# Kernel tuning notes

Measured on AMD Instinct MI355X. Metric: run time of the kernel, lower is better.

The kernel has to match this reference:

```python
import jax, jax.numpy as jnp
import numpy as np

B, P, D = 8, 1024, 1024
H, N = 16, 64  # num_heads, head_dim


def setup_inputs() -> dict:
    key = jax.random.key(0)
    k1, k2, k3 = jax.random.split(key, 3)
    inputs = jax.random.normal(k1, (B, P, D), dtype=jnp.float32)
    # Keras 'random_normal' initializer: stddev 0.05
    w_qkv = jax.random.normal(k2, (H, 3, D, N), dtype=jnp.float32) * 0.05
    w_o = jax.random.normal(k3, (N * H, D), dtype=jnp.float32) * 0.05
    return {"inputs": inputs, "w_qkv": w_qkv, "w_o": w_o}


def reference(inputs, w_qkv, w_o):
    # Per-head QKV projection: [b,p,d] x [h,3,d,n] -> [b,h,3,p,n]
    proj = jnp.einsum('bpv,havn->bhapn', inputs, w_qkv)
    q = proj[:, :, 0]  # [b,h,p,n]
    k = proj[:, :, 1]
    v = proj[:, :, 2]
    head_dim = q.shape[-1]
    scale = 1.0 / jnp.sqrt(jnp.asarray(head_dim, dtype=jnp.float32))
    scores = jnp.einsum('bhqn,bhkn->bhqk', q, k) * scale  # [b,h,p,p]
    attn = jax.nn.softmax(scores, axis=-1)
    out = jnp.einsum('bhqk,bhkn->bhqn', attn, v)  # [b,h,p,n]
    # concat heads along feature dim: [b,p,h*n]
    b, h, p, n = out.shape
    concat = out.transpose(0, 2, 1, 3).reshape(b, p, h * n)
    return jnp.einsum('bpi,ij->bpj', concat, w_o)  # [b,p,d_model]
```

## Files before the change

### kernel.cpp

```cpp
#include <hip/hip_runtime.h>
#include <stdint.h>

typedef _Float16 f16;
typedef __attribute__((ext_vector_type(4))) _Float16 f16x4;
typedef __attribute__((ext_vector_type(8))) _Float16 f16x8;
typedef __attribute__((ext_vector_type(4))) float f32x4;

__device__ __forceinline__ void gload_lds16(const void* g, void* l) {
  __builtin_amdgcn_global_load_lds(
      (__attribute__((address_space(1))) void*)const_cast<void*>(g),
      (__attribute__((address_space(3))) void*)l, 16, 0, 0);
}


__global__ void convert_x(const float* __restrict__ in, f16* __restrict__ out) {
  int i = blockIdx.x * 256 + threadIdx.x;
  float4 v = ((const float4*)in)[i];
  f16x4 hv;
  hv[0] = (f16)v.x; hv[1] = (f16)v.y; hv[2] = (f16)v.z; hv[3] = (f16)v.w;
  ((f16x4*)out)[i] = hv;
}

__global__ void transpose_wqkv(const float* __restrict__ in, f16* __restrict__ out) {
  __shared__ float tile[64][65];
  int s = blockIdx.x >> 4;
  int vt = blockIdx.x & 15;
  int tx = threadIdx.x & 63, ty = threadIdx.x >> 6;
#pragma unroll
  for (int i = 0; i < 16; i++) {
    int r = i * 4 + ty;
    tile[r][tx] = in[((size_t)(s * 1024 + vt * 64 + r)) * 64 + tx];
  }
  __syncthreads();
#pragma unroll
  for (int i = 0; i < 16; i++) {
    int n = i * 4 + ty;
    out[((size_t)(s * 64 + n)) * 1024 + vt * 64 + tx] = (f16)tile[tx][n];
  }
}

__global__ void transpose_wo(const float* __restrict__ in, f16* __restrict__ out) {
  __shared__ float tile[64][65];
  int rt = blockIdx.x >> 4, ct = blockIdx.x & 15;
  int tx = threadIdx.x & 63, ty = threadIdx.x >> 6;
#pragma unroll
  for (int i = 0; i < 16; i++) {
    int r = i * 4 + ty;
    tile[r][tx] = in[((size_t)(rt * 64 + r)) * 1024 + ct * 64 + tx];
  }
  __syncthreads();
#pragma unroll
  for (int i = 0; i < 16; i++) {
    int j = i * 4 + ty;
    out[((size_t)(ct * 64 + j)) * 1024 + rt * 64 + tx] = (f16)tile[tx][j];
  }
}

__global__ void transpose_v(const f16* __restrict__ QKV, f16* __restrict__ VT) {
  __shared__ f16 tile[64][65];
  int bh = blockIdx.x >> 4, pt = blockIdx.x & 15;
  int b = bh >> 4, h = bh & 15;
  int tx = threadIdx.x & 63, ty = threadIdx.x >> 6;
#pragma unroll
  for (int i = 0; i < 16; i++) {
    int r = i * 4 + ty;
    tile[r][tx] = QKV[((size_t)(b * 1024 + pt * 64 + r)) * 3072 + h * 192 + 128 + tx];
  }
  __syncthreads();
#pragma unroll
  for (int i = 0; i < 16; i++) {
    int n = i * 4 + ty;
    VT[((size_t)(bh * 64 + n)) * 1024 + pt * 64 + tx] = tile[tx][n];
  }
}

template <int OUTMODE>
__global__ __launch_bounds__(256, 2) void gemm_kernel(
    const f16* __restrict__ A, const f16* __restrict__ BT, void* __restrict__ out,
    int M, int N, int K) {
  __shared__ __align__(16) f16 As[128][32];
  __shared__ __align__(16) f16 Bs[128][32];
  const int t = threadIdx.x;
  const int lane = t & 63, wave = t >> 6;
  const int lr = lane & 15, lg = lane >> 4;
  const int wm = wave >> 1, wn = wave & 1;
  const int nTN = N >> 7;
  const int bm = blockIdx.x / nTN, bn = blockIdx.x % nTN;
  const f16* Ab = A + (size_t)bm * 128 * K;
  const f16* Bb = BT + (size_t)bn * 128 * K;

  const f32x4 zero4 = {0.f, 0.f, 0.f, 0.f};
  f32x4 acc[4][4];
#pragma unroll
  for (int m = 0; m < 4; m++)
#pragma unroll
    for (int n = 0; n < 4; n++) acc[m][n] = zero4;

  for (int k0 = 0; k0 < K; k0 += 32) {
    __syncthreads();
#pragma unroll
    for (int i = 0; i < 2; i++) {
      int q = wave * 2 + i;
      int e = q * 64 + lane;
      int r = e >> 2, bi = e & 3;
      gload_lds16(Ab + (size_t)r * K + k0 + ((bi ^ (r & 3)) << 3),
                  (char*)&As[0][0] + q * 1024);
      gload_lds16(Bb + (size_t)r * K + k0 + ((bi ^ (r & 3)) << 3),
                  (char*)&Bs[0][0] + q * 1024);
    }
    __syncthreads();
    f16x8 af[4], bf[4];
#pragma unroll
    for (int m = 0; m < 4; m++) {
      int r = wm * 64 + m * 16 + lr;
      af[m] = *(const f16x8*)&As[r][(lg ^ (r & 3)) << 3];
    }
#pragma unroll
    for (int n = 0; n < 4; n++) {
      int r = wn * 64 + n * 16 + lr;
      bf[n] = *(const f16x8*)&Bs[r][(lg ^ (r & 3)) << 3];
    }
#pragma unroll
    for (int m = 0; m < 4; m++)
#pragma unroll
      for (int n = 0; n < 4; n++)
        acc[m][n] = __builtin_amdgcn_mfma_f32_16x16x32_f16(af[m], bf[n], acc[m][n], 0, 0, 0);
  }

  const int r0 = bm * 128 + wm * 64;
  const int c0 = bn * 128 + wn * 64;
#pragma unroll
  for (int m = 0; m < 4; m++)
#pragma unroll
    for (int n = 0; n < 4; n++)
#pragma unroll
      for (int i = 0; i < 4; i++) {
        int gr = r0 + m * 16 + lg * 4 + i;
        int gc = c0 + n * 16 + lr;
        if (OUTMODE == 0)
          ((f16*)out)[(size_t)gr * N + gc] = (f16)acc[m][n][i];
        else
          ((float*)out)[(size_t)gr * N + gc] = acc[m][n][i];
      }
}

__global__ __launch_bounds__(256, 3) void attn_kernel(
    const f16* __restrict__ QKV, const f16* __restrict__ VT, f16* __restrict__ C) {
  __shared__ __align__(16) f16 smem[8192];

  const int t = threadIdx.x, lane = t & 63, wave = t >> 6;
  const int lr = lane & 15, lg = lane >> 4;
  const int pt = blockIdx.x, bh = blockIdx.y;
  const int b = bh >> 4, h = bh & 15;
  const int p0 = pt * 128;

  const f16* Qg = QKV + ((size_t)(b * 1024 + p0)) * 3072 + h * 192;
  const f16* Kg = QKV + ((size_t)(b * 1024)) * 3072 + h * 192 + 64;
  const f16* Vg = VT + (size_t)bh * 64 * 1024;

#pragma unroll
  for (int i = 0; i < 4; i++) {
    int q = wave * 4 + i;
    int u = q * 64 + lane;
    int r = u >> 3, j = u & 7;
    gload_lds16(Qg + (size_t)r * 3072 + ((j ^ (r & 7)) << 3), (char*)smem + q * 1024);
  }
  __syncthreads();

  f16x8 qa[2][2];
#pragma unroll
  for (int m = 0; m < 2; m++)
#pragma unroll
    for (int hh = 0; hh < 2; hh++) {
      int r = wave * 32 + m * 16 + lr;
      qa[m][hh] = *(const f16x8*)&smem[(size_t)r * 64 + (((hh * 4 + lg) ^ (lr & 7)) << 3)];
    }
  __syncthreads();

  const f32x4 zero4 = {0.f, 0.f, 0.f, 0.f};
  f32x4 o[2][4];
#pragma unroll
  for (int m = 0; m < 2; m++)
#pragma unroll
    for (int n = 0; n < 4; n++) o[m][n] = zero4;
  float mrun[2] = {-1e30f, -1e30f};
  float lrun[2] = {0.f, 0.f};

#pragma unroll 1
  for (int kc = 0; kc < 16; kc++) {
#pragma unroll
    for (int i = 0; i < 2; i++) {
      int q = wave * 2 + i;
      int u = q * 64 + lane;
      int r = u >> 3, j = u & 7;
      gload_lds16(Kg + (size_t)(kc * 64 + r) * 3072 + ((j ^ (r & 7)) << 3),
                  (char*)smem + q * 1024);
      gload_lds16(Vg + (size_t)r * 1024 + kc * 64 + ((j ^ (r & 7)) << 3),
                  (char*)smem + 8192 + q * 1024);
    }
    __syncthreads();

    f32x4 s[2][4];
#pragma unroll
    for (int m = 0; m < 2; m++)
#pragma unroll
      for (int kb = 0; kb < 4; kb++) s[m][kb] = zero4;
#pragma unroll
    for (int kb = 0; kb < 4; kb++) {
      int r = kb * 16 + lr;
      f16x8 kf0 = *(const f16x8*)&smem[(size_t)r * 64 + ((lg ^ (lr & 7)) << 3)];
      f16x8 kf1 = *(const f16x8*)&smem[(size_t)r * 64 + (((4 + lg) ^ (lr & 7)) << 3)];
#pragma unroll
      for (int m = 0; m < 2; m++) {
        s[m][kb] = __builtin_amdgcn_mfma_f32_16x16x32_f16(kf0, qa[m][0], s[m][kb], 0, 0, 0);
        s[m][kb] = __builtin_amdgcn_mfma_f32_16x16x32_f16(kf1, qa[m][1], s[m][kb], 0, 0, 0);
      }
    }

    f16x4 pa[2][4];
#pragma unroll
    for (int m = 0; m < 2; m++) {
      float mx = s[m][0][0];
#pragma unroll
      for (int kb = 0; kb < 4; kb++)
#pragma unroll
        for (int i = 0; i < 4; i++) mx = fmaxf(mx, s[m][kb][i]);
      mx = fmaxf(mx, __shfl_xor(mx, 16));
      mx = fmaxf(mx, __shfl_xor(mx, 32));
      mx *= 0.125f;
      if (__any(mx > mrun[m] + 3.0f)) {
        float mnew = fmaxf(mrun[m], mx);
        float alpha = __expf(mrun[m] - mnew);
        mrun[m] = mnew;
        lrun[m] *= alpha;
#pragma unroll
        for (int i = 0; i < 4; i++) {
          float ai = __shfl(alpha, (lane & 48) | (lg * 4 + i));
#pragma unroll
          for (int n = 0; n < 4; n++) o[m][n][i] *= ai;
        }
      }
      float mt = mrun[m] * 1.44269504f;
      float rs = 0.f;
#pragma unroll
      for (int kb = 0; kb < 4; kb++)
#pragma unroll
        for (int i = 0; i < 4; i++) {
          float p = exp2f(fmaf(s[m][kb][i], 0.180336878f, -mt));
          rs += p;
          pa[m][kb][i] = (f16)p;
        }
      rs += __shfl_xor(rs, 16);
      rs += __shfl_xor(rs, 32);
      lrun[m] += rs;
    }

#pragma unroll
    for (int n = 0; n < 4; n++) {
#pragma unroll
      for (int kb = 0; kb < 4; kb++) {
        const f16x4 vb = *(const f16x4*)((const char*)smem + 8192 + (size_t)(n * 16 + lr) * 128 +
                                         ((((kb * 2 + (lg >> 1)) ^ (lr & 7)) << 4) | ((lg & 1) << 3)));
        o[0][n] = __builtin_amdgcn_mfma_f32_16x16x16f16(pa[0][kb], vb, o[0][n], 0, 0, 0);
        o[1][n] = __builtin_amdgcn_mfma_f32_16x16x16f16(pa[1][kb], vb, o[1][n], 0, 0, 0);
      }
    }
    __syncthreads();
  }

#pragma unroll
  for (int m = 0; m < 2; m++) {
    float linv = 1.f / lrun[m];
#pragma unroll
    for (int i = 0; i < 4; i++) {
      float li = __shfl(linv, (lane & 48) | (lg * 4 + i));
      int prow = p0 + wave * 32 + m * 16 + lg * 4 + i;
#pragma unroll
      for (int n = 0; n < 4; n++) {
        int col = h * 64 + n * 16 + lr;
        C[((size_t)(b * 1024 + prow)) * 1024 + col] = (f16)(o[m][n][i] * li);
      }
    }
  }
}

extern "C" void kernel_launch(void* const* d_in, const int* in_sizes, int n_in,
                              void* d_out, int out_size, void* d_ws, size_t ws_size,
                              hipStream_t stream) {
  const float* X = (const float*)d_in[0];
  const float* Wqkv = (const float*)d_in[1];
  const float* Wo = (const float*)d_in[2];
  float* Y = (float*)d_out;

  f16* ws = (f16*)d_ws;
  f16* X16 = ws;
  f16* WqkvT = ws + 8388608;
  f16* WoT = ws + 11534336;
  f16* QKV = ws + 12582912;
  f16* VT = (f16*)d_out;

  convert_x<<<8192, 256, 0, stream>>>(X, X16);
  transpose_wqkv<<<768, 256, 0, stream>>>(Wqkv, WqkvT);
  transpose_wo<<<256, 256, 0, stream>>>(Wo, WoT);
  gemm_kernel<0><<<64 * 24, 256, 0, stream>>>(X16, WqkvT, QKV, 8192, 3072, 1024);
  transpose_v<<<2048, 256, 0, stream>>>(QKV, VT);
  attn_kernel<<<dim3(8, 128), 256, 0, stream>>>(QKV, VT, X16 );
  gemm_kernel<1><<<64 * 8, 256, 0, stream>>>(X16 , WoT, Y, 8192, 1024, 1024);
}
```

Measured before the change: 194.9 us.

## Fuse V transpose into QKV GEMM epilogue and double-buffer attention K/V tiles

The QKV weight layout is reordered to [q|k|v][head][dim], so the QKV GEMM epilogue can write V directly in transposed per-head layout. That removes the separate transpose_v kernel and its extra read/write pass. The attention kernel now double-buffers K/V tiles in LDS, prefetching two chunks ahead, and wraps the MFMA sections in s_setprio. It also uses a tree max reduction and raises launch bounds to 4 blocks per SM. The cost is doubled LDS per block (32 KB) and more register and occupancy pressure, and the strided f16x4 V stores from the GEMM epilogue may be poorly coalesced.

```diff
diff --git a/kernel.cpp b/kernel.cpp
--- a/kernel.cpp
+++ b/kernel.cpp
@@ -25,6 +25,7 @@
   __shared__ float tile[64][65];
   int s = blockIdx.x >> 4;
   int vt = blockIdx.x & 15;
+  int hh = s / 3, a = s - hh * 3;
   int tx = threadIdx.x & 63, ty = threadIdx.x >> 6;
 #pragma unroll
   for (int i = 0; i < 16; i++) {
@@ -35,7 +36,7 @@
 #pragma unroll
   for (int i = 0; i < 16; i++) {
     int n = i * 4 + ty;
-    out[((size_t)(s * 64 + n)) * 1024 + vt * 64 + tx] = (f16)tile[tx][n];
+    out[((size_t)(a * 1024 + hh * 64 + n)) * 1024 + vt * 64 + tx] = (f16)tile[tx][n];
   }
 }
 
@@ -56,28 +57,10 @@
   }
 }
 
-__global__ void transpose_v(const f16* __restrict__ QKV, f16* __restrict__ VT) {
-  __shared__ f16 tile[64][65];
-  int bh = blockIdx.x >> 4, pt = blockIdx.x & 15;
-  int b = bh >> 4, h = bh & 15;
-  int tx = threadIdx.x & 63, ty = threadIdx.x >> 6;
-#pragma unroll
-  for (int i = 0; i < 16; i++) {
-    int r = i * 4 + ty;
-    tile[r][tx] = QKV[((size_t)(b * 1024 + pt * 64 + r)) * 3072 + h * 192 + 128 + tx];
-  }
-  __syncthreads();
-#pragma unroll
-  for (int i = 0; i < 16; i++) {
-    int n = i * 4 + ty;
-    VT[((size_t)(bh * 64 + n)) * 1024 + pt * 64 + tx] = tile[tx][n];
-  }
-}
-
 template <int OUTMODE>
 __global__ __launch_bounds__(256, 2) void gemm_kernel(
     const f16* __restrict__ A, const f16* __restrict__ BT, void* __restrict__ out,
-    int M, int N, int K) {
+    void* __restrict__ out2, int M, int N, int K) {
   __shared__ __align__(16) f16 As[128][32];
   __shared__ __align__(16) f16 Bs[128][32];
   const int t = threadIdx.x;
@@ -129,24 +112,42 @@
 
   const int r0 = bm * 128 + wm * 64;
   const int c0 = bn * 128 + wn * 64;
-#pragma unroll
-  for (int m = 0; m < 4; m++)
-#pragma unroll
-    for (int n = 0; n < 4; n++)
-#pragma unroll
-      for (int i = 0; i < 4; i++) {
-        int gr = r0 + m * 16 + lg * 4 + i;
-        int gc = c0 + n * 16 + lr;
-        if (OUTMODE == 0)
-          ((f16*)out)[(size_t)gr * N + gc] = (f16)acc[m][n][i];
-        else
-          ((float*)out)[(size_t)gr * N + gc] = acc[m][n][i];
-      }
-}
-
-__global__ __launch_bounds__(256, 3) void attn_kernel(
+  if (OUTMODE == 2 && bn >= 16) {
+    f16* VT = (f16*)out2;
+    const int bb = bm >> 3;
+#pragma unroll
+    for (int m = 0; m < 4; m++) {
+      int p = r0 + m * 16 + lg * 4;
+      int pl = p & 1023;
+#pragma unroll
+      for (int n = 0; n < 4; n++) {
+        int vcol = c0 - 2048 + n * 16 + lr;
+        f16x4 pv;
+#pragma unroll
+        for (int i = 0; i < 4; i++) pv[i] = (f16)acc[m][n][i];
+        *(f16x4*)&VT[((size_t)(bb * 16 + (vcol >> 6)) * 64 + (vcol & 63)) * 1024 + pl] = pv;
+      }
+    }
+  } else {
+#pragma unroll
+    for (int m = 0; m < 4; m++)
+#pragma unroll
+      for (int n = 0; n < 4; n++)
+#pragma unroll
+        for (int i = 0; i < 4; i++) {
+          int gr = r0 + m * 16 + lg * 4 + i;
+          int gc = c0 + n * 16 + lr;
+          if (OUTMODE == 1)
+            ((float*)out)[(size_t)gr * N + gc] = acc[m][n][i];
+          else
+            ((f16*)out)[(size_t)gr * N + gc] = (f16)acc[m][n][i];
+        }
+  }
+}
+
+__global__ __launch_bounds__(256, 4) void attn_kernel(
     const f16* __restrict__ QKV, const f16* __restrict__ VT, f16* __restrict__ C) {
-  __shared__ __align__(16) f16 smem[8192];
+  __shared__ __align__(16) f16 smem[16384];
 
   const int t = threadIdx.x, lane = t & 63, wave = t >> 6;
   const int lr = lane & 15, lg = lane >> 4;
@@ -154,8 +155,8 @@
   const int b = bh >> 4, h = bh & 15;
   const int p0 = pt * 128;
 
-  const f16* Qg = QKV + ((size_t)(b * 1024 + p0)) * 3072 + h * 192;
-  const f16* Kg = QKV + ((size_t)(b * 1024)) * 3072 + h * 192 + 64;
+  const f16* Qg = QKV + ((size_t)(b * 1024 + p0)) * 3072 + h * 64;
+  const f16* Kg = QKV + ((size_t)(b * 1024)) * 3072 + 1024 + h * 64;
   const f16* Vg = VT + (size_t)bh * 64 * 1024;
 
 #pragma unroll
@@ -177,54 +178,65 @@
     }
   __syncthreads();
 
-  const f32x4 zero4 = {0.f, 0.f, 0.f, 0.f};
-  f32x4 o[2][4];
-#pragma unroll
-  for (int m = 0; m < 2; m++)
-#pragma unroll
-    for (int n = 0; n < 4; n++) o[m][n] = zero4;
-  float mrun[2] = {-1e30f, -1e30f};
-  float lrun[2] = {0.f, 0.f};
-
-#pragma unroll 1
-  for (int kc = 0; kc < 16; kc++) {
+  auto STAGE = [&](int kc, int cur) {
 #pragma unroll
     for (int i = 0; i < 2; i++) {
       int q = wave * 2 + i;
       int u = q * 64 + lane;
       int r = u >> 3, j = u & 7;
       gload_lds16(Kg + (size_t)(kc * 64 + r) * 3072 + ((j ^ (r & 7)) << 3),
-                  (char*)smem + q * 1024);
+                  (char*)smem + cur * 16384 + q * 1024);
       gload_lds16(Vg + (size_t)r * 1024 + kc * 64 + ((j ^ (r & 7)) << 3),
-                  (char*)smem + 8192 + q * 1024);
-    }
-    __syncthreads();
+                  (char*)smem + cur * 16384 + 8192 + q * 1024);
+    }
+  };
+
+  STAGE(0, 0);
+  STAGE(1, 1);
+  __syncthreads();
+
+  const f32x4 zero4 = {0.f, 0.f, 0.f, 0.f};
+  f32x4 o[2][4];
+#pragma unroll
+  for (int m = 0; m < 2; m++)
+#pragma unroll
+    for (int n = 0; n < 4; n++) o[m][n] = zero4;
+  float mrun[2] = {-1e30f, -1e30f};
+  float lrun[2] = {0.f, 0.f};
+
+#pragma unroll 1
+  for (int kc = 0; kc < 16; kc++) {
+    const int cur = kc & 1;
+    const int kB = cur * 8192;
+    const char* vB = (const char*)smem + cur * 16384 + 8192;
 
     f32x4 s[2][4];
 #pragma unroll
     for (int m = 0; m < 2; m++)
 #pragma unroll
       for (int kb = 0; kb < 4; kb++) s[m][kb] = zero4;
+    __builtin_amdgcn_s_setprio(1);
 #pragma unroll
     for (int kb = 0; kb < 4; kb++) {
       int r = kb * 16 + lr;
-      f16x8 kf0 = *(const f16x8*)&smem[(size_t)r * 64 + ((lg ^ (lr & 7)) << 3)];
-      f16x8 kf1 = *(const f16x8*)&smem[(size_t)r * 64 + (((4 + lg) ^ (lr & 7)) << 3)];
+      f16x8 kf0 = *(const f16x8*)&smem[kB + (size_t)r * 64 + ((lg ^ (lr & 7)) << 3)];
+      f16x8 kf1 = *(const f16x8*)&smem[kB + (size_t)r * 64 + (((4 + lg) ^ (lr & 7)) << 3)];
 #pragma unroll
       for (int m = 0; m < 2; m++) {
         s[m][kb] = __builtin_amdgcn_mfma_f32_16x16x32_f16(kf0, qa[m][0], s[m][kb], 0, 0, 0);
         s[m][kb] = __builtin_amdgcn_mfma_f32_16x16x32_f16(kf1, qa[m][1], s[m][kb], 0, 0, 0);
       }
     }
+    __builtin_amdgcn_s_setprio(0);
 
     f16x4 pa[2][4];
 #pragma unroll
     for (int m = 0; m < 2; m++) {
-      float mx = s[m][0][0];
-#pragma unroll
-      for (int kb = 0; kb < 4; kb++)
-#pragma unroll
-        for (int i = 0; i < 4; i++) mx = fmaxf(mx, s[m][kb][i]);
+      float mx01 = fmaxf(fmaxf(s[m][0][0], s[m][0][1]), fmaxf(s[m][0][2], s[m][0][3]));
+      float mx23 = fmaxf(fmaxf(s[m][1][0], s[m][1][1]), fmaxf(s[m][1][2], s[m][1][3]));
+      float mx45 = fmaxf(fmaxf(s[m][2][0], s[m][2][1]), fmaxf(s[m][2][2], s[m][2][3]));
+      float mx67 = fmaxf(fmaxf(s[m][3][0], s[m][3][1]), fmaxf(s[m][3][2], s[m][3][3]));
+      float mx = fmaxf(fmaxf(mx01, mx23), fmaxf(mx45, mx67));
       mx = fmaxf(mx, __shfl_xor(mx, 16));
       mx = fmaxf(mx, __shfl_xor(mx, 32));
       mx *= 0.125f;
@@ -255,17 +267,21 @@
       lrun[m] += rs;
     }
 
+    __builtin_amdgcn_s_setprio(1);
 #pragma unroll
     for (int n = 0; n < 4; n++) {
 #pragma unroll
       for (int kb = 0; kb < 4; kb++) {
-        const f16x4 vb = *(const f16x4*)((const char*)smem + 8192 + (size_t)(n * 16 + lr) * 128 +
+        const f16x4 vb = *(const f16x4*)(vB + (size_t)(n * 16 + lr) * 128 +
                                          ((((kb * 2 + (lg >> 1)) ^ (lr & 7)) << 4) | ((lg & 1) << 3)));
         o[0][n] = __builtin_amdgcn_mfma_f32_16x16x16f16(pa[0][kb], vb, o[0][n], 0, 0, 0);
         o[1][n] = __builtin_amdgcn_mfma_f32_16x16x16f16(pa[1][kb], vb, o[1][n], 0, 0, 0);
       }
     }
+    __builtin_amdgcn_s_setprio(0);
+
     __syncthreads();
+    if (kc + 2 < 16) STAGE(kc + 2, cur);
   }
 
 #pragma unroll
@@ -302,8 +318,7 @@
   convert_x<<<8192, 256, 0, stream>>>(X, X16);
   transpose_wqkv<<<768, 256, 0, stream>>>(Wqkv, WqkvT);
   transpose_wo<<<256, 256, 0, stream>>>(Wo, WoT);
-  gemm_kernel<0><<<64 * 24, 256, 0, stream>>>(X16, WqkvT, QKV, 8192, 3072, 1024);
-  transpose_v<<<2048, 256, 0, stream>>>(QKV, VT);
+  gemm_kernel<2><<<64 * 24, 256, 0, stream>>>(X16, WqkvT, QKV, VT, 8192, 3072, 1024);
   attn_kernel<<<dim3(8, 128), 256, 0, stream>>>(QKV, VT, X16 );
-  gemm_kernel<1><<<64 * 8, 256, 0, stream>>>(X16 , WoT, Y, 8192, 1024, 1024);
-}
+  gemm_kernel<1><<<64 * 8, 256, 0, stream>>>(X16 , WoT, Y, nullptr, 8192, 1024, 1024);
+}
```

Measured after the change: 192.0 us. No clear change (-1.5%).
